# Optimization experiments

Measured on AMD Instinct MI355X. Metric: run time of the kernel, lower is better.

## Reference

```python
import jax, jax.numpy as jnp
from jax import lax
import numpy as np

IMG = 500
FM = 31
RATIOS = [1.0, 2.0, 0.5]
SCALES = [128, 256, 512]
PRE_NMS = 6000
POST_NMS = 1500  # train_nms_topn (test=False)
IOU_THR = 0.7
VARIANCES = np.array([0.1, 0.1, 0.2, 0.2], np.float32)
BATCH = 16


def _gen_anchors():
    # bbox_utils.generate_anchors: normalized [y1,x1,y2,x2], grid of 31x31 centers,
    # 9 base shapes from (scale, ratio), clipped to [0,1].
    ctr = (np.arange(FM, dtype=np.float32) + 0.5) / FM
    cy, cx = np.meshgrid(ctr, ctr, indexing='ij')          # [FM,FM]
    base = []
    for s in SCALES:
        for r in RATIOS:
            w = s * np.sqrt(r) / IMG
            h = s / np.sqrt(r) / IMG
            base.append([h, w])
    base = np.array(base, np.float32)                       # [9,2]
    h, w = base[:, 0], base[:, 1]
    cy = cy[..., None]; cx = cx[..., None]                  # [FM,FM,1]
    anc = np.stack([cy - h / 2, cx - w / 2, cy + h / 2, cx + w / 2], axis=-1)
    return np.clip(anc.reshape(-1, 4), 0.0, 1.0).astype(np.float32)  # [8649,4]


def setup_inputs() -> dict:
    key = jax.random.key(0)
    k1, k2 = jax.random.split(key)
    return {
        'rpn_bbox_deltas': jax.random.normal(k1, (BATCH, FM, FM, 36), jnp.float32),
        'rpn_probs': jax.random.uniform(k2, (BATCH, FM, FM, 9), jnp.float32),
        'anchors': jnp.asarray(_gen_anchors()),
    }


def _nms_keep(boxes, scores):
    # Greedy NMS over score-descending-sorted boxes; returns keep mask [N].
    N = boxes.shape[0]
    y1, x1, y2, x2 = boxes[:, 0], boxes[:, 1], boxes[:, 2], boxes[:, 3]
    area = (y2 - y1) * (x2 - x1)

    def body(i, state):
        supp, keep, cnt = state
        valid = jnp.logical_and(jnp.logical_not(supp[i]), cnt < POST_NMS)
        keep = keep.at[i].set(valid)
        cnt = cnt + valid.astype(jnp.int32)
        ih = jnp.maximum(jnp.minimum(y2[i], y2) - jnp.maximum(y1[i], y1), 0.0)
        iw = jnp.maximum(jnp.minimum(x2[i], x2) - jnp.maximum(x1[i], x1), 0.0)
        inter = ih * iw
        iou = inter / (area[i] + area - inter + 1e-8)
        supp = jnp.where(valid, jnp.logical_or(supp, iou > IOU_THR), supp)
        return supp, keep, cnt

    supp0 = jnp.zeros((N,), bool)
    keep0 = jnp.zeros((N,), bool)
    _, keep, _ = lax.fori_loop(0, N, body, (supp0, keep0, jnp.int32(0)))
    return keep


def reference(rpn_bbox_deltas, rpn_probs, anchors):
    B = rpn_bbox_deltas.shape[0]
    N = anchors.shape[0]
    deltas = rpn_bbox_deltas.reshape(B, N, 4) * jnp.asarray(VARIANCES)  # [B,N,4]
    probs = rpn_probs.reshape(B, N)                                     # [B,N]

    # decode anchor deltas -> boxes
    anc_h = anchors[:, 2] - anchors[:, 0]
    anc_w = anchors[:, 3] - anchors[:, 1]
    ctr_y = anchors[:, 0] + 0.5 * anc_h
    ctr_x = anchors[:, 1] + 0.5 * anc_w
    bh = jnp.exp(deltas[..., 2]) * anc_h
    bw = jnp.exp(deltas[..., 3]) * anc_w
    bcy = deltas[..., 0] * anc_h + ctr_y
    bcx = deltas[..., 1] * anc_w + ctr_x
    y1 = bcy - 0.5 * bh
    x1 = bcx - 0.5 * bw
    boxes = jnp.stack([y1, x1, y1 + bh, x1 + bw], axis=-1)              # [B,N,4]

    # pre-NMS top-k by objectness (sorted descending)
    top_scores, top_idx = lax.top_k(probs, PRE_NMS)                     # [B,PRE_NMS]
    top_boxes = jnp.take_along_axis(boxes, top_idx[..., None], axis=1)  # [B,PRE_NMS,4]

    # greedy NMS (selection is non-differentiable, compute on stopped values)
    keep = jax.vmap(_nms_keep)(lax.stop_gradient(top_boxes),
                               lax.stop_gradient(top_scores))           # [B,PRE_NMS] bool

    # compact kept entries to the front, zero-pad to POST_NMS (combined NMS semantics)
    rank = jnp.cumsum(keep, axis=1) - 1
    slot = jnp.where(keep, rank, POST_NMS)  # dropped entries go to overflow slot

    def _scatter(sl, bx, sc, k):
        ob = jnp.zeros((POST_NMS + 1, 4), bx.dtype).at[sl].set(jnp.where(k[:, None], bx, 0.0))
        os = jnp.zeros((POST_NMS + 1,), sc.dtype).at[sl].set(jnp.where(k, sc, 0.0))
        return ob[:POST_NMS], os[:POST_NMS]

    roi_bboxes, roi_scores = jax.vmap(_scatter)(slot, top_boxes, top_scores, keep)
    roi_bboxes = jnp.clip(roi_bboxes, 0.0, 1.0)  # clip_boxes=True in combined NMS
    return roi_bboxes, roi_scores
```

## Files before the change

kernel.cpp:

```cpp
#include <hip/hip_runtime.h>
#include <hip/hip_bf16.h>

#define BATCH   16
#define N_ANC   8649
#define SORT_N  16384
#define PRE     6000
#define POST    1500
#define ROWW    188
#define MROWS   6016
#define NGRP    188
#define GQUADS  1504
#define TI      256
#define TJ      256

__global__ __launch_bounds__(256) void k_decode(
    const float* __restrict__ deltas, const float* __restrict__ probs,
    const float* __restrict__ anchors, float4* __restrict__ boxes,
    unsigned long long* __restrict__ keys)
{
    int t = blockIdx.x * 256 + threadIdx.x;
    if (t >= BATCH * SORT_N) return;
    int b = t / SORT_N;
    int n = t - b * SORT_N;
    if (n >= N_ANC) { keys[t] = ~0ULL; return; }

    float s = probs[(size_t)b * N_ANC + n];
    unsigned int bits = __float_as_uint(s);
    unsigned int u = bits ^ ((bits & 0x80000000u) ? 0xFFFFFFFFu : 0x80000000u);
    keys[(size_t)b * SORT_N + n] = ((unsigned long long)(~u) << 32) | (unsigned int)n;

    float4 a = ((const float4*)anchors)[n];
    float4 d = ((const float4*)deltas)[(size_t)b * N_ANC + n];
    float dy = d.x * 0.1f, dx = d.y * 0.1f, dh = d.z * 0.2f, dw = d.w * 0.2f;
    float ah = a.z - a.x, aw = a.w - a.y;
    float cy = a.x + 0.5f * ah, cx = a.y + 0.5f * aw;
    float bh = expf(dh) * ah, bw = expf(dw) * aw;
    float bcy = dy * ah + cy, bcx = dx * aw + cx;
    float y1 = bcy - 0.5f * bh, x1 = bcx - 0.5f * bw;
    boxes[(size_t)b * N_ANC + n] = make_float4(y1, x1, y1 + bh, x1 + bw);
}

__global__ __launch_bounds__(1024) void k_sort_chunk(unsigned long long* __restrict__ keys)
{
    __shared__ unsigned long long sb[8192];
    int b = blockIdx.x >> 1;
    int c = blockIdx.x & 1;
    unsigned long long* g = keys + (size_t)b * SORT_N + c * 8192;

    for (int t = threadIdx.x; t < 8192; t += 1024) sb[t] = g[t];
    __syncthreads();
    for (int k = 2; k <= 8192; k <<= 1) {
        for (int j = k >> 1; j >= 1; j >>= 1) {
            for (int p = threadIdx.x; p < 4096; p += 1024) {
                int i  = ((p & ~(j - 1)) << 1) | (p & (j - 1));
                int gi = (c << 13) | i;
                bool asc = ((gi & k) == 0);
                unsigned long long a = sb[i], b2 = sb[i | j];
                bool sw = asc ? (a > b2) : (a < b2);
                if (sw) { sb[i] = b2; sb[i | j] = a; }
            }
            __syncthreads();
        }
    }
    for (int t = threadIdx.x; t < 8192; t += 1024) g[t] = sb[t];
}

__global__ __launch_bounds__(1024) void k_sort_merge(unsigned long long* __restrict__ keys)
{
    __shared__ unsigned long long sb[8192];
    int b = blockIdx.x;
    unsigned long long* kb = keys + (size_t)b * SORT_N;

    for (int p = threadIdx.x; p < 8192; p += 1024) {
        unsigned long long a = kb[p], b2 = kb[p + 8192];
        if (a > b2) { kb[p] = b2; kb[p + 8192] = a; }
    }
    __syncthreads();

    for (int t = threadIdx.x; t < 8192; t += 1024) sb[t] = kb[t];
    __syncthreads();
    for (int j = 4096; j >= 1; j >>= 1) {
        for (int p = threadIdx.x; p < 4096; p += 1024) {
            int i = ((p & ~(j - 1)) << 1) | (p & (j - 1));
            unsigned long long a = sb[i], b2 = sb[i | j];
            if (a > b2) { sb[i] = b2; sb[i | j] = a; }
        }
        __syncthreads();
    }
    for (int t = threadIdx.x; t < 6016; t += 1024) kb[t] = sb[t];
}

__global__ __launch_bounds__(256) void k_gather(
    const unsigned long long* __restrict__ keys, const float4* __restrict__ boxes,
    const float* __restrict__ probs,
    float4* __restrict__ sboxes, float* __restrict__ sscores)
{
    int t = blockIdx.x * 256 + threadIdx.x;
    if (t >= BATCH * PRE) return;
    int b = t / PRE;
    int r = t - b * PRE;
    unsigned long long k = keys[(size_t)b * SORT_N + r];
    int idx = (int)(k & 0xFFFFFFFFu);
    sboxes[(size_t)b * PRE + r]  = boxes[(size_t)b * N_ANC + idx];
    sscores[(size_t)b * PRE + r] = probs[(size_t)b * N_ANC + idx];
}

__global__ __launch_bounds__(256) void k_iou(
    const float4* __restrict__ sboxes, unsigned int* __restrict__ mask)
{
    int it = blockIdx.x;
    int jt = blockIdx.y;
    int b  = blockIdx.z;
    if (jt < it) return;

    __shared__ float4 jb[TJ];
    __shared__ float  ja[TJ];
    int t = threadIdx.x;
    int j = jt * TJ + t;
    float4 bj = (j < PRE) ? sboxes[(size_t)b * PRE + j]
                          : make_float4(-2e6f, -2e6f, -1.5e6f, -1.5e6f);
    jb[t] = bj;
    ja[t] = (bj.z - bj.x) * (bj.w - bj.y);
    __syncthreads();

    int i = it * TI + t;
    if (i >= PRE) return;
    float4 bi = sboxes[(size_t)b * PRE + i];
    float areai = (bi.z - bi.x) * (bi.w - bi.y);

    unsigned int w[8];
    if (jt > it) {
        for (int wq = 0; wq < 8; wq++) {
            unsigned int bits = 0u;
            #pragma unroll
            for (int jj = 0; jj < 32; jj++) {
                int lj = wq * 32 + jj;
                float4 bx = jb[lj];
                float ih = fmaxf(fminf(bi.z, bx.z) - fmaxf(bi.x, bx.x), 0.0f);
                float iw = fmaxf(fminf(bi.w, bx.w) - fmaxf(bi.y, bx.y), 0.0f);
                float inter = ih * iw;
                float iou = inter / (areai + ja[lj] - inter + 1e-8f);
                if (iou > 0.7f) bits |= (1u << jj);
            }
            w[wq] = bits;
        }
    } else {
        for (int wq = 0; wq < 8; wq++) {
            int jbase = jt * TJ + wq * 32;
            unsigned int bits = 0u;
            if (jbase + 31 > i) {
                #pragma unroll
                for (int jj = 0; jj < 32; jj++) {
                    int lj = wq * 32 + jj;
                    float4 bx = jb[lj];
                    float ih = fmaxf(fminf(bi.z, bx.z) - fmaxf(bi.x, bx.x), 0.0f);
                    float iw = fmaxf(fminf(bi.w, bx.w) - fmaxf(bi.y, bx.y), 0.0f);
                    float inter = ih * iw;
                    float iou = inter / (areai + ja[lj] - inter + 1e-8f);
                    if (iou > 0.7f && (jbase + jj) > i) bits |= (1u << jj);
                }
            }
            w[wq] = bits;
        }
    }

    unsigned int* row = mask + ((size_t)b * MROWS + i) * ROWW + jt * 8;
    ((uint4*)row)[0] = make_uint4(w[0], w[1], w[2], w[3]);
    if (jt < 23) ((uint4*)row)[1] = make_uint4(w[4], w[5], w[6], w[7]);
}

__global__ __launch_bounds__(256, 1) void k_scan(
    const unsigned int* __restrict__ mask,
    int* __restrict__ out_idx, int* __restrict__ out_cnt)
{
    __shared__ unsigned int rows[2][32 * ROWW];
    __shared__ unsigned int sw_lds[2];
    int b   = blockIdx.x;
    int tid = threadIdx.x;
    const uint4* mb = (const uint4*)(mask + (size_t)b * MROWS * ROWW);

    if (tid < 2) sw_lds[tid] = 0u;

    uint4 sreg[6];
    #pragma unroll
    for (int i = 0; i < 6; i++) {
        int q = tid + i * 256;
        sreg[i] = (q < GQUADS) ? mb[q] : make_uint4(0, 0, 0, 0);
    }
    #pragma unroll
    for (int i = 0; i < 6; i++) {
        int q = tid + i * 256;
        if (q < GQUADS) ((uint4*)rows[0])[q] = sreg[i];
    }
    __syncthreads();

    unsigned int st_word = 0u;
    int cnt = 0;
    int* oi = out_idx + b * POST;

    for (int g = 0; g < NGRP; g++) {
        int cur = g & 1;
        bool have_next = (g + 1 < NGRP);

        if (have_next) {
            const uint4* src = mb + (size_t)(g + 1) * GQUADS;
            #pragma unroll
            for (int i = 0; i < 6; i++) {
                int q = tid + i * 256;
                sreg[i] = (q < GQUADS) ? src[q] : make_uint4(0, 0, 0, 0);
            }
        }

        unsigned int tri[32];
        #pragma unroll
        for (int k = 0; k < 32; k++) tri[k] = rows[cur][k * ROWW + g];

        unsigned int sw = sw_lds[cur];

        int need_n = POST - cnt;
        unsigned int valid = (g == NGRP - 1) ? 0xFFFFu : 0xFFFFFFFFu;
        unsigned int alive = ~sw & valid;
        unsigned int km2 = 0u;
        int cum = 0;
        #pragma unroll
        for (int k = 0; k < 32; k++) {
            unsigned int bit = (alive >> k) & 1u;
            bit &= (cum < need_n) ? 1u : 0u;
            cum += (int)bit;
            km2 |= bit << k;
            alive &= ~((0u - bit) & tri[k]);
        }

        if (tid < 32 && ((km2 >> tid) & 1u))
            oi[cnt + __popc(km2 & ((1u << tid) - 1u))] = g * 32 + tid;
        cnt += cum;

        if (tid < ROWW) {
            unsigned int acc = 0u;
            #pragma unroll
            for (int k = 0; k < 32; k++)
                acc |= rows[cur][k * ROWW + tid] & (0u - ((km2 >> k) & 1u));
            st_word |= acc;
        }

        if (have_next && tid == g + 1) sw_lds[(g + 1) & 1] = st_word;

        if (have_next) {
            uint4* dst = (uint4*)rows[cur ^ 1];
            #pragma unroll
            for (int i = 0; i < 6; i++) {
                int q = tid + i * 256;
                if (q < GQUADS) dst[q] = sreg[i];
            }
        }
        __syncthreads();
    }
    if (tid == 0) out_cnt[b] = cnt;
}

__global__ __launch_bounds__(256) void k_out(
    const float4* __restrict__ sboxes, const float* __restrict__ sscores,
    const int* __restrict__ out_idx, const int* __restrict__ out_cnt,
    float* __restrict__ out)
{
    int t = blockIdx.x * 256 + threadIdx.x;
    if (t >= BATCH * POST) return;
    int b = t / POST;
    int r = t - b * POST;
    float4 v = make_float4(0, 0, 0, 0);
    float sc = 0.f;
    if (r < out_cnt[b]) {
        int i = out_idx[b * POST + r];
        float4 bx = sboxes[(size_t)b * PRE + i];
        v.x = fminf(fmaxf(bx.x, 0.f), 1.f);
        v.y = fminf(fmaxf(bx.y, 0.f), 1.f);
        v.z = fminf(fmaxf(bx.z, 0.f), 1.f);
        v.w = fminf(fmaxf(bx.w, 0.f), 1.f);
        sc = sscores[(size_t)b * PRE + i];
    }
    ((float4*)out)[t] = v;
    out[(size_t)BATCH * POST * 4 + t] = sc;
}

extern "C" void kernel_launch(void* const* d_in, const int* in_sizes, int n_in,
                              void* d_out, int out_size, void* d_ws, size_t ws_size,
                              hipStream_t stream)
{
    const float* deltas  = (const float*)d_in[0];
    const float* probs   = (const float*)d_in[1];
    const float* anchors = (const float*)d_in[2];
    float* out = (float*)d_out;

    char* ws = (char*)d_ws;
    size_t off = 0;
    auto alloc = [&](size_t bytes) {
        size_t o = off;
        off = (off + bytes + 255) & ~(size_t)255;
        return o;
    };
    float4* boxes            = (float4*)(ws + alloc((size_t)BATCH * N_ANC * 16));
    unsigned long long* keys = (unsigned long long*)(ws + alloc((size_t)BATCH * SORT_N * 8));
    float4* sboxes           = (float4*)(ws + alloc((size_t)BATCH * PRE * 16));
    float* sscores           = (float*)(ws + alloc((size_t)BATCH * PRE * 4));
    unsigned int* mask       = (unsigned int*)(ws + alloc((size_t)BATCH * MROWS * ROWW * 4));
    int* oidx                = (int*)(ws + alloc((size_t)BATCH * POST * 4));
    int* ocnt                = (int*)(ws + alloc((size_t)BATCH * 4));

    k_decode<<<(BATCH * SORT_N + 255) / 256, 256, 0, stream>>>(deltas, probs, anchors, boxes, keys);
    k_sort_chunk<<<BATCH * 2, 1024, 0, stream>>>(keys);
    k_sort_merge<<<BATCH, 1024, 0, stream>>>(keys);
    k_gather<<<(BATCH * PRE + 255) / 256, 256, 0, stream>>>(keys, boxes, probs, sboxes, sscores);
    k_iou<<<dim3(24, 24, BATCH), 256, 0, stream>>>(sboxes, mask);
    k_scan<<<BATCH, 256, 0, stream>>>(mask, oidx, ocnt);
    k_out<<<(BATCH * POST + 255) / 256, 256, 0, stream>>>(sboxes, sscores, oidx, ocnt, out);
}
```

Baseline: 694.3 us.

## Fuse decode into sort, output into scan, and retile IoU with two rows per thread

Box decode and key construction move into the chunk-sort kernel, which removes one launch and the global round-trip of the keys. The output compaction moves into the scan kernel through a shared-memory kept list. The IoU kernel now computes two i-rows per thread over 512-row tiles, and it replaces the divide with a reciprocal plus an exact fallback near the threshold. The scan takes a cheaper path without the count limit and redoes the limited pass only when the group would overflow the post-NMS limit. These changes reduce launches and per-element arithmetic, at the cost of more registers in the IoU kernel and longer serial work in the scan.

```diff
diff --git a/kernel.cpp b/kernel.cpp
--- a/kernel.cpp
+++ b/kernel.cpp
@@ -10,45 +10,40 @@
 #define MROWS   6016
 #define NGRP    188
 #define GQUADS  1504
-#define TI      256
-#define TJ      256
-
-__global__ __launch_bounds__(256) void k_decode(
+
+__global__ __launch_bounds__(1024) void k_sortdecode(
     const float* __restrict__ deltas, const float* __restrict__ probs,
     const float* __restrict__ anchors, float4* __restrict__ boxes,
     unsigned long long* __restrict__ keys)
 {
-    int t = blockIdx.x * 256 + threadIdx.x;
-    if (t >= BATCH * SORT_N) return;
-    int b = t / SORT_N;
-    int n = t - b * SORT_N;
-    if (n >= N_ANC) { keys[t] = ~0ULL; return; }
-
-    float s = probs[(size_t)b * N_ANC + n];
-    unsigned int bits = __float_as_uint(s);
-    unsigned int u = bits ^ ((bits & 0x80000000u) ? 0xFFFFFFFFu : 0x80000000u);
-    keys[(size_t)b * SORT_N + n] = ((unsigned long long)(~u) << 32) | (unsigned int)n;
-
-    float4 a = ((const float4*)anchors)[n];
-    float4 d = ((const float4*)deltas)[(size_t)b * N_ANC + n];
-    float dy = d.x * 0.1f, dx = d.y * 0.1f, dh = d.z * 0.2f, dw = d.w * 0.2f;
-    float ah = a.z - a.x, aw = a.w - a.y;
-    float cy = a.x + 0.5f * ah, cx = a.y + 0.5f * aw;
-    float bh = expf(dh) * ah, bw = expf(dw) * aw;
-    float bcy = dy * ah + cy, bcx = dx * aw + cx;
-    float y1 = bcy - 0.5f * bh, x1 = bcx - 0.5f * bw;
-    boxes[(size_t)b * N_ANC + n] = make_float4(y1, x1, y1 + bh, x1 + bw);
-}
-
-__global__ __launch_bounds__(1024) void k_sort_chunk(unsigned long long* __restrict__ keys)
-{
     __shared__ unsigned long long sb[8192];
     int b = blockIdx.x >> 1;
     int c = blockIdx.x & 1;
-    unsigned long long* g = keys + (size_t)b * SORT_N + c * 8192;
-
-    for (int t = threadIdx.x; t < 8192; t += 1024) sb[t] = g[t];
-    __syncthreads();
+    int base = c * 8192;
+
+    for (int i = threadIdx.x; i < 8192; i += 1024) {
+        int n = base + i;
+        unsigned long long key = ~0ULL;
+        if (n < N_ANC) {
+            float s = probs[(size_t)b * N_ANC + n];
+            unsigned int bits = __float_as_uint(s);
+            unsigned int u = bits ^ ((bits & 0x80000000u) ? 0xFFFFFFFFu : 0x80000000u);
+            key = ((unsigned long long)(~u) << 32) | (unsigned int)n;
+
+            float4 a = ((const float4*)anchors)[n];
+            float4 d = ((const float4*)deltas)[(size_t)b * N_ANC + n];
+            float dy = d.x * 0.1f, dx = d.y * 0.1f, dh = d.z * 0.2f, dw = d.w * 0.2f;
+            float ah = a.z - a.x, aw = a.w - a.y;
+            float cy = a.x + 0.5f * ah, cx = a.y + 0.5f * aw;
+            float bh = expf(dh) * ah, bw = expf(dw) * aw;
+            float bcy = dy * ah + cy, bcx = dx * aw + cx;
+            float y1 = bcy - 0.5f * bh, x1 = bcx - 0.5f * bw;
+            boxes[(size_t)b * N_ANC + n] = make_float4(y1, x1, y1 + bh, x1 + bw);
+        }
+        sb[i] = key;
+    }
+    __syncthreads();
+
     for (int k = 2; k <= 8192; k <<= 1) {
         for (int j = k >> 1; j >= 1; j >>= 1) {
             for (int p = threadIdx.x; p < 4096; p += 1024) {
@@ -62,6 +57,7 @@
             __syncthreads();
         }
     }
+    unsigned long long* g = keys + (size_t)b * SORT_N + base;
     for (int t = threadIdx.x; t < 8192; t += 1024) g[t] = sb[t];
 }
 
@@ -105,76 +101,97 @@
     sscores[(size_t)b * PRE + r] = probs[(size_t)b * N_ANC + idx];
 }
 
+template<bool PRED>
+__device__ __forceinline__ unsigned int iou_word(
+    const float4* __restrict__ jb, const float* __restrict__ ja,
+    int wq, float4 bi, float ai, int trow)
+{
+    unsigned int bits = 0u;
+    #pragma unroll
+    for (int jj = 0; jj < 32; jj++) {
+        int lj = wq * 32 + jj;
+        float4 bx = jb[lj];
+        float ih = fmaxf(fminf(bi.z, bx.z) - fmaxf(bi.x, bx.x), 0.0f);
+        float iw = fmaxf(fminf(bi.w, bx.w) - fmaxf(bi.y, bx.y), 0.0f);
+        float inter = ih * iw;
+        float denom = ai + ja[lj] - inter + 1e-8f;
+        float ap = inter * __builtin_amdgcn_rcpf(denom);
+        float d = ap - 0.7f;
+        bool set;
+        if (fabsf(d) < 1e-6f) set = (inter / denom > 0.7f);
+        else                  set = (d > 0.0f);
+        if (PRED) set = set && (lj > trow);
+        if (set) bits |= (1u << jj);
+    }
+    return bits;
+}
+
 __global__ __launch_bounds__(256) void k_iou(
     const float4* __restrict__ sboxes, unsigned int* __restrict__ mask)
 {
     int it = blockIdx.x;
     int jt = blockIdx.y;
     int b  = blockIdx.z;
-    if (jt < it) return;
-
-    __shared__ float4 jb[TJ];
-    __shared__ float  ja[TJ];
+    int ibase  = it << 9;
+    int jbase0 = jt << 8;
+    if (jbase0 < ibase) return;
+
+    __shared__ float4 jb[256];
+    __shared__ float  ja[256];
     int t = threadIdx.x;
-    int j = jt * TJ + t;
+    int j = jbase0 + t;
     float4 bj = (j < PRE) ? sboxes[(size_t)b * PRE + j]
                           : make_float4(-2e6f, -2e6f, -1.5e6f, -1.5e6f);
     jb[t] = bj;
     ja[t] = (bj.z - bj.x) * (bj.w - bj.y);
     __syncthreads();
 
-    int i = it * TI + t;
-    if (i >= PRE) return;
-    float4 bi = sboxes[(size_t)b * PRE + i];
-    float areai = (bi.z - bi.x) * (bi.w - bi.y);
-
-    unsigned int w[8];
-    if (jt > it) {
+    int i0 = ibase + t;
+    int i1 = ibase + 256 + t;
+    bool do1 = (jbase0 >= ibase + 256);
+
+    float4 b0 = (i0 < PRE) ? sboxes[(size_t)b * PRE + i0] : make_float4(0, 0, 0, 0);
+    float  a0 = (b0.z - b0.x) * (b0.w - b0.y);
+    float4 b1 = (do1 && i1 < PRE) ? sboxes[(size_t)b * PRE + i1] : make_float4(0, 0, 0, 0);
+    float  a1 = (b1.z - b1.x) * (b1.w - b1.y);
+
+    unsigned int w0[8], w1[8];
+    if (jbase0 == ibase) {
+        #pragma unroll
+        for (int wq = 0; wq < 8; wq++) w0[wq] = iou_word<true>(jb, ja, wq, b0, a0, t);
+    } else if (jbase0 == ibase + 256) {
+        #pragma unroll
         for (int wq = 0; wq < 8; wq++) {
-            unsigned int bits = 0u;
-            #pragma unroll
-            for (int jj = 0; jj < 32; jj++) {
-                int lj = wq * 32 + jj;
-                float4 bx = jb[lj];
-                float ih = fmaxf(fminf(bi.z, bx.z) - fmaxf(bi.x, bx.x), 0.0f);
-                float iw = fmaxf(fminf(bi.w, bx.w) - fmaxf(bi.y, bx.y), 0.0f);
-                float inter = ih * iw;
-                float iou = inter / (areai + ja[lj] - inter + 1e-8f);
-                if (iou > 0.7f) bits |= (1u << jj);
-            }
-            w[wq] = bits;
+            w0[wq] = iou_word<false>(jb, ja, wq, b0, a0, 0);
+            w1[wq] = iou_word<true>(jb, ja, wq, b1, a1, t);
         }
     } else {
+        #pragma unroll
         for (int wq = 0; wq < 8; wq++) {
-            int jbase = jt * TJ + wq * 32;
-            unsigned int bits = 0u;
-            if (jbase + 31 > i) {
-                #pragma unroll
-                for (int jj = 0; jj < 32; jj++) {
-                    int lj = wq * 32 + jj;
-                    float4 bx = jb[lj];
-                    float ih = fmaxf(fminf(bi.z, bx.z) - fmaxf(bi.x, bx.x), 0.0f);
-                    float iw = fmaxf(fminf(bi.w, bx.w) - fmaxf(bi.y, bx.y), 0.0f);
-                    float inter = ih * iw;
-                    float iou = inter / (areai + ja[lj] - inter + 1e-8f);
-                    if (iou > 0.7f && (jbase + jj) > i) bits |= (1u << jj);
-                }
-            }
-            w[wq] = bits;
-        }
-    }
-
-    unsigned int* row = mask + ((size_t)b * MROWS + i) * ROWW + jt * 8;
-    ((uint4*)row)[0] = make_uint4(w[0], w[1], w[2], w[3]);
-    if (jt < 23) ((uint4*)row)[1] = make_uint4(w[4], w[5], w[6], w[7]);
+            w0[wq] = iou_word<false>(jb, ja, wq, b0, a0, 0);
+            w1[wq] = iou_word<false>(jb, ja, wq, b1, a1, 0);
+        }
+    }
+
+    if (i0 < PRE) {
+        unsigned int* row = mask + ((size_t)b * MROWS + i0) * ROWW + jt * 8;
+        ((uint4*)row)[0] = make_uint4(w0[0], w0[1], w0[2], w0[3]);
+        if (jt < 23) ((uint4*)row)[1] = make_uint4(w0[4], w0[5], w0[6], w0[7]);
+    }
+    if (do1 && i1 < PRE) {
+        unsigned int* row = mask + ((size_t)b * MROWS + i1) * ROWW + jt * 8;
+        ((uint4*)row)[0] = make_uint4(w1[0], w1[1], w1[2], w1[3]);
+        if (jt < 23) ((uint4*)row)[1] = make_uint4(w1[4], w1[5], w1[6], w1[7]);
+    }
 }
 
 __global__ __launch_bounds__(256, 1) void k_scan(
-    const unsigned int* __restrict__ mask,
-    int* __restrict__ out_idx, int* __restrict__ out_cnt)
+    const unsigned int* __restrict__ mask, const float4* __restrict__ sboxes,
+    const float* __restrict__ sscores, float* __restrict__ out)
 {
     __shared__ unsigned int rows[2][32 * ROWW];
     __shared__ unsigned int sw_lds[2];
+    __shared__ int kept_lds[POST];
     int b   = blockIdx.x;
     int tid = threadIdx.x;
     const uint4* mb = (const uint4*)(mask + (size_t)b * MROWS * ROWW);
@@ -196,7 +213,6 @@
 
     unsigned int st_word = 0u;
     int cnt = 0;
-    int* oi = out_idx + b * POST;
 
     for (int g = 0; g < NGRP; g++) {
         int cur = g & 1;
@@ -220,26 +236,35 @@
         int need_n = POST - cnt;
         unsigned int valid = (g == NGRP - 1) ? 0xFFFFu : 0xFFFFFFFFu;
         unsigned int alive = ~sw & valid;
-        unsigned int km2 = 0u;
-        int cum = 0;
+        unsigned int km = 0u;
         #pragma unroll
         for (int k = 0; k < 32; k++) {
             unsigned int bit = (alive >> k) & 1u;
-            bit &= (cum < need_n) ? 1u : 0u;
-            cum += (int)bit;
-            km2 |= bit << k;
+            km |= bit << k;
             alive &= ~((0u - bit) & tri[k]);
         }
-
-        if (tid < 32 && ((km2 >> tid) & 1u))
-            oi[cnt + __popc(km2 & ((1u << tid) - 1u))] = g * 32 + tid;
-        cnt += cum;
+        int kc = __popc(km);
+        if (kc > need_n) {
+            alive = ~sw & valid; km = 0u; kc = 0;
+            #pragma unroll
+            for (int k = 0; k < 32; k++) {
+                unsigned int bit = (alive >> k) & 1u;
+                bit &= (kc < need_n) ? 1u : 0u;
+                kc += (int)bit;
+                km |= bit << k;
+                alive &= ~((0u - bit) & tri[k]);
+            }
+        }
+
+        if (tid < 32 && ((km >> tid) & 1u))
+            kept_lds[cnt + __popc(km & ((1u << tid) - 1u))] = g * 32 + tid;
+        cnt += kc;
 
         if (tid < ROWW) {
             unsigned int acc = 0u;
             #pragma unroll
             for (int k = 0; k < 32; k++)
-                acc |= rows[cur][k * ROWW + tid] & (0u - ((km2 >> k) & 1u));
+                acc |= rows[cur][k * ROWW + tid] & (0u - ((km >> k) & 1u));
             st_word |= acc;
         }
 
@@ -255,31 +280,22 @@
         }
         __syncthreads();
     }
-    if (tid == 0) out_cnt[b] = cnt;
-}
-
-__global__ __launch_bounds__(256) void k_out(
-    const float4* __restrict__ sboxes, const float* __restrict__ sscores,
-    const int* __restrict__ out_idx, const int* __restrict__ out_cnt,
-    float* __restrict__ out)
-{
-    int t = blockIdx.x * 256 + threadIdx.x;
-    if (t >= BATCH * POST) return;
-    int b = t / POST;
-    int r = t - b * POST;
-    float4 v = make_float4(0, 0, 0, 0);
-    float sc = 0.f;
-    if (r < out_cnt[b]) {
-        int i = out_idx[b * POST + r];
-        float4 bx = sboxes[(size_t)b * PRE + i];
-        v.x = fminf(fmaxf(bx.x, 0.f), 1.f);
-        v.y = fminf(fmaxf(bx.y, 0.f), 1.f);
-        v.z = fminf(fmaxf(bx.z, 0.f), 1.f);
-        v.w = fminf(fmaxf(bx.w, 0.f), 1.f);
-        sc = sscores[(size_t)b * PRE + i];
-    }
-    ((float4*)out)[t] = v;
-    out[(size_t)BATCH * POST * 4 + t] = sc;
+
+    for (int r = tid; r < POST; r += 256) {
+        float4 v = make_float4(0, 0, 0, 0);
+        float sc = 0.f;
+        if (r < cnt) {
+            int i = kept_lds[r];
+            float4 bx = sboxes[(size_t)b * PRE + i];
+            v.x = fminf(fmaxf(bx.x, 0.f), 1.f);
+            v.y = fminf(fmaxf(bx.y, 0.f), 1.f);
+            v.z = fminf(fmaxf(bx.z, 0.f), 1.f);
+            v.w = fminf(fmaxf(bx.w, 0.f), 1.f);
+            sc = sscores[(size_t)b * PRE + i];
+        }
+        ((float4*)out)[(size_t)b * POST + r] = v;
+        out[(size_t)BATCH * POST * 4 + (size_t)b * POST + r] = sc;
+    }
 }
 
 extern "C" void kernel_launch(void* const* d_in, const int* in_sizes, int n_in,
@@ -303,14 +319,10 @@
     float4* sboxes           = (float4*)(ws + alloc((size_t)BATCH * PRE * 16));
     float* sscores           = (float*)(ws + alloc((size_t)BATCH * PRE * 4));
     unsigned int* mask       = (unsigned int*)(ws + alloc((size_t)BATCH * MROWS * ROWW * 4));
-    int* oidx                = (int*)(ws + alloc((size_t)BATCH * POST * 4));
-    int* ocnt                = (int*)(ws + alloc((size_t)BATCH * 4));
-
-    k_decode<<<(BATCH * SORT_N + 255) / 256, 256, 0, stream>>>(deltas, probs, anchors, boxes, keys);
-    k_sort_chunk<<<BATCH * 2, 1024, 0, stream>>>(keys);
+
+    k_sortdecode<<<BATCH * 2, 1024, 0, stream>>>(deltas, probs, anchors, boxes, keys);
     k_sort_merge<<<BATCH, 1024, 0, stream>>>(keys);
     k_gather<<<(BATCH * PRE + 255) / 256, 256, 0, stream>>>(keys, boxes, probs, sboxes, sscores);
-    k_iou<<<dim3(24, 24, BATCH), 256, 0, stream>>>(sboxes, mask);
-    k_scan<<<BATCH, 256, 0, stream>>>(mask, oidx, ocnt);
-    k_out<<<(BATCH * POST + 255) / 256, 256, 0, stream>>>(sboxes, sscores, oidx, ocnt, out);
-}
+    k_iou<<<dim3(12, 24, BATCH), 256, 0, stream>>>(sboxes, mask);
+    k_scan<<<BATCH, 256, 0, stream>>>(mask, sboxes, sscores, out);
+}
```

Result: slower. 889.8 us (+28.2%).
